# Kernel optimization log

Measured on AMD Instinct MI355X. Metric: run time of the kernel, lower is better.

Reference implementation:

```python
import jax, jax.numpy as jnp
import numpy as np

N = 50000   # nodes
E = 800000  # edges (before self-loops)
IN, HID, OUT = 128, 128, 64


def gcn_norm(edge_index, num_nodes):
    # add self loops with weight 1, then symmetric deg^-1/2 normalization
    loop = jnp.arange(num_nodes, dtype=edge_index.dtype)
    row = jnp.concatenate([edge_index[0], loop])
    col = jnp.concatenate([edge_index[1], loop])
    ew = jnp.ones(row.shape[0], dtype=jnp.float32)
    deg = jax.ops.segment_sum(ew, col, num_segments=num_nodes)
    dis = jnp.where(deg > 0, jax.lax.rsqrt(deg), 0.0)
    norm = dis[row] * ew * dis[col]
    return row, col, norm


def gcn_conv(x, row, col, norm, W, b):
    h = x @ W                                   # [N, F_out] dense GEMM
    msg = h[row] * norm[:, None]                # gather + scale over edges
    out = jax.ops.segment_sum(msg, col, num_segments=x.shape[0])  # scatter-add
    return out + b


def setup_inputs() -> dict:
    key = jax.random.key(0)
    k0, k1, k2, k3, k4, k5 = jax.random.split(key, 6)
    x = jax.random.normal(k0, (N, IN), dtype=jnp.float32)
    edge_index = jax.random.randint(k1, (2, E), 0, N, dtype=jnp.int32)
    # glorot-style init for linear weights, zeros for bias (PyG default)
    W1 = jax.random.normal(k2, (IN, HID), dtype=jnp.float32) * np.float32(np.sqrt(1.0 / IN))
    b1 = jnp.zeros((HID,), dtype=jnp.float32)
    W2 = jax.random.normal(k3, (HID, OUT), dtype=jnp.float32) * np.float32(np.sqrt(1.0 / HID))
    b2 = jnp.zeros((OUT,), dtype=jnp.float32)
    return {"x": x, "edge_index": edge_index, "W1": W1, "b1": b1, "W2": W2, "b2": b2}


def reference(x, edge_index, W1, b1, W2, b2):
    row, col, norm = gcn_norm(edge_index, x.shape[0])
    h = jax.nn.relu(gcn_conv(x, row, col, norm, W1, b1))
    # dropout is a no-op in eval mode (training=False)
    out = gcn_conv(h, row, col, norm, W2, b2)
    return out
```

## Files before the change

kernel.cpp:

```cpp
#include <hip/hip_runtime.h>
#include <hip/hip_fp16.h>


#define Nn 50000
#define Ne 800000
#define SCAN_B ((Nn + 1023) / 1024)

using f16x8 = _Float16 __attribute__((ext_vector_type(8)));
using f32x4 = float __attribute__((ext_vector_type(4)));

__global__ __launch_bounds__(256) void k_count(const int* __restrict__ col,
                                               int* __restrict__ degi,
                                               unsigned short* __restrict__ rank) {
  int e = blockIdx.x * 256 + threadIdx.x;
  if (e < Ne) rank[e] = (unsigned short)atomicAdd(&degi[col[e]], 1);
}

__global__ __launch_bounds__(1024) void k_scan1(const int* __restrict__ degi,
                                                int* __restrict__ rowptr,
                                                float* __restrict__ dis,
                                                int* __restrict__ bsum) {
  __shared__ int wsum[16];
  int tid = threadIdx.x;
  int lane = tid & 63, wid = tid >> 6;
  int i = blockIdx.x * 1024 + tid;
  int v = (i < Nn) ? degi[i] : 0;
  if (i < Nn) dis[i] = rsqrtf((float)(v + 1));
  int incl = v;
  #pragma unroll
  for (int off = 1; off < 64; off <<= 1) {
    int t = __shfl_up(incl, off);
    if (lane >= off) incl += t;
  }
  if (lane == 63) wsum[wid] = incl;
  __syncthreads();
  if (wid == 0) {
    int wv = (lane < 16) ? wsum[lane] : 0;
    #pragma unroll
    for (int off = 1; off < 16; off <<= 1) {
      int t = __shfl_up(wv, off);
      if (lane >= off) wv += t;
    }
    if (lane < 16) wsum[lane] = wv;
  }
  __syncthreads();
  int woff = (wid > 0) ? wsum[wid - 1] : 0;
  if (i < Nn) rowptr[i] = woff + incl - v;
  if (tid == 0) bsum[blockIdx.x] = wsum[15];
}

__global__ __launch_bounds__(64) void k_scan2(int* __restrict__ bsum,
                                              int* __restrict__ rowptr) {
  int lane = threadIdx.x;
  int v = (lane < SCAN_B) ? bsum[lane] : 0;
  int incl = v;
  #pragma unroll
  for (int off = 1; off < 64; off <<= 1) {
    int t = __shfl_up(incl, off);
    if (lane >= off) incl += t;
  }
  if (lane < SCAN_B) bsum[lane] = incl - v;
  if (lane == 63) rowptr[Nn] = incl;
}

__global__ __launch_bounds__(1024) void k_scan3(int* __restrict__ rowptr,
                                                const int* __restrict__ bsum) {
  int i = blockIdx.x * 1024 + threadIdx.x;
  if (i < Nn) rowptr[i] += bsum[blockIdx.x];
}

__global__ __launch_bounds__(256) void k_fill(const int* __restrict__ row,
                                              const int* __restrict__ col,
                                              const float* __restrict__ dis,
                                              const int* __restrict__ rowptr,
                                              const unsigned short* __restrict__ rank,
                                              unsigned int* __restrict__ csr) {
  int e = blockIdx.x * 256 + threadIdx.x;
  if (e >= Ne) return;
  int r = row[e], c = col[e];
  int pos = rowptr[c] + (int)rank[e];
  __half hn = __float2half(dis[r] * dis[c]);
  csr[pos] = ((unsigned int)__half_as_ushort(hn) << 16) | (unsigned int)r;
}

template <int LDO>
__global__ __launch_bounds__(256) void k_gemm_mfma(const float* __restrict__ X,
                                                   const float* __restrict__ W,
                                                   __half* __restrict__ H, int n) {
  __shared__ _Float16 Xs[64 * 136];
  __shared__ _Float16 Wts[LDO * 136];
  const int tid = threadIdx.x;
  const int base = blockIdx.x * 64;

  {
    constexpr int C4 = LDO / 4;
    for (int idx4 = tid; idx4 < 32 * LDO; idx4 += 256) {
      int k = idx4 / C4;
      int c = (idx4 % C4) * 4;
      float4 wv = ((const float4*)W)[idx4];
      Wts[(c + 0) * 136 + k] = (_Float16)wv.x;
      Wts[(c + 1) * 136 + k] = (_Float16)wv.y;
      Wts[(c + 2) * 136 + k] = (_Float16)wv.z;
      Wts[(c + 3) * 136 + k] = (_Float16)wv.w;
    }
  }
  {
    for (int u = tid; u < 64 * 16; u += 256) {
      int r = u >> 4, seg = u & 15;
      int node = base + r;
      if (node >= n) node = n - 1;
      const float4* xg = (const float4*)(X + (size_t)node * 128 + seg * 8);
      float4 x0 = xg[0], x1 = xg[1];
      f16x8 hv;
      hv[0] = (_Float16)x0.x; hv[1] = (_Float16)x0.y;
      hv[2] = (_Float16)x0.z; hv[3] = (_Float16)x0.w;
      hv[4] = (_Float16)x1.x; hv[5] = (_Float16)x1.y;
      hv[6] = (_Float16)x1.z; hv[7] = (_Float16)x1.w;
      *(f16x8*)&Xs[r * 136 + seg * 8] = hv;
    }
  }
  __syncthreads();

  const int w = tid >> 6, lane = tid & 63;
  const int quad = lane >> 4, mrow = lane & 15;
  constexpr int NCT = LDO / 16;

  f32x4 acc[NCT];
  #pragma unroll
  for (int ct = 0; ct < NCT; ++ct) acc[ct] = (f32x4){0.f, 0.f, 0.f, 0.f};

  #pragma unroll
  for (int ko = 0; ko < 4; ++ko) {
    f16x8 av = *(const f16x8*)&Xs[(w * 16 + mrow) * 136 + ko * 32 + quad * 8];
    #pragma unroll
    for (int ct = 0; ct < NCT; ++ct) {
      f16x8 bv = *(const f16x8*)&Wts[(ct * 16 + mrow) * 136 + ko * 32 + quad * 8];
      acc[ct] = __builtin_amdgcn_mfma_f32_16x16x32_f16(av, bv, acc[ct], 0, 0, 0);
    }
  }

  #pragma unroll
  for (int ct = 0; ct < NCT; ++ct) {
    #pragma unroll
    for (int r = 0; r < 4; ++r) {
      int node = base + w * 16 + quad * 4 + r;
      if (node < n)
        H[(size_t)node * LDO + ct * 16 + mrow] = __float2half(acc[ct][r]);
    }
  }
}

__device__ __forceinline__ float2 h2f(unsigned int u) {
  return __half22float2(*(const __half2*)&u);
}
__device__ __forceinline__ float wdec(unsigned int u) {
  return __half2float(__ushort_as_half((unsigned short)(u >> 16)));
}

__global__ __launch_bounds__(256) void k_agg128(const __half* __restrict__ H,
                                                const unsigned int* __restrict__ csr,
                                                const int* __restrict__ rowptr,
                                                const float* __restrict__ dis,
                                                const float* __restrict__ bias,
                                                float* __restrict__ Out, int n) {
  const int wid = threadIdx.x >> 6, lane = threadIdx.x & 63;
  const int sub = lane >> 4, fl = lane & 15;
  int v = blockIdx.x * 16 + wid * 4 + sub;
  if (v >= n) return;
  int s = rowptr[v], e = rowptr[v + 1];
  float d = dis[v];
  float sw = d * d;
  const uint4* Hq = (const uint4*)H;
  uint4 hv = Hq[(size_t)v * 16 + fl];
  float2 p0 = h2f(hv.x), p1 = h2f(hv.y), p2 = h2f(hv.z), p3 = h2f(hv.w);
  float a0 = p0.x * sw, a1 = p0.y * sw, a2 = p1.x * sw, a3 = p1.y * sw;
  float a4 = p2.x * sw, a5 = p2.y * sw, a6 = p3.x * sw, a7 = p3.y * sw;
  int i = s;
  for (; i + 4 <= e; i += 4) {
    unsigned int u0 = csr[i + 0], u1 = csr[i + 1];
    unsigned int u2 = csr[i + 2], u3 = csr[i + 3];
    uint4 q0 = Hq[(size_t)(u0 & 0xFFFFu) * 16 + fl];
    uint4 q1 = Hq[(size_t)(u1 & 0xFFFFu) * 16 + fl];
    uint4 q2 = Hq[(size_t)(u2 & 0xFFFFu) * 16 + fl];
    uint4 q3 = Hq[(size_t)(u3 & 0xFFFFu) * 16 + fl];
    float w0 = wdec(u0), w1 = wdec(u1), w2 = wdec(u2), w3 = wdec(u3);
    float2 t;
    t = h2f(q0.x); a0 = fmaf(w0, t.x, a0); a1 = fmaf(w0, t.y, a1);
    t = h2f(q0.y); a2 = fmaf(w0, t.x, a2); a3 = fmaf(w0, t.y, a3);
    t = h2f(q0.z); a4 = fmaf(w0, t.x, a4); a5 = fmaf(w0, t.y, a5);
    t = h2f(q0.w); a6 = fmaf(w0, t.x, a6); a7 = fmaf(w0, t.y, a7);
    t = h2f(q1.x); a0 = fmaf(w1, t.x, a0); a1 = fmaf(w1, t.y, a1);
    t = h2f(q1.y); a2 = fmaf(w1, t.x, a2); a3 = fmaf(w1, t.y, a3);
    t = h2f(q1.z); a4 = fmaf(w1, t.x, a4); a5 = fmaf(w1, t.y, a5);
    t = h2f(q1.w); a6 = fmaf(w1, t.x, a6); a7 = fmaf(w1, t.y, a7);
    t = h2f(q2.x); a0 = fmaf(w2, t.x, a0); a1 = fmaf(w2, t.y, a1);
    t = h2f(q2.y); a2 = fmaf(w2, t.x, a2); a3 = fmaf(w2, t.y, a3);
    t = h2f(q2.z); a4 = fmaf(w2, t.x, a4); a5 = fmaf(w2, t.y, a5);
    t = h2f(q2.w); a6 = fmaf(w2, t.x, a6); a7 = fmaf(w2, t.y, a7);
    t = h2f(q3.x); a0 = fmaf(w3, t.x, a0); a1 = fmaf(w3, t.y, a1);
    t = h2f(q3.y); a2 = fmaf(w3, t.x, a2); a3 = fmaf(w3, t.y, a3);
    t = h2f(q3.z); a4 = fmaf(w3, t.x, a4); a5 = fmaf(w3, t.y, a5);
    t = h2f(q3.w); a6 = fmaf(w3, t.x, a6); a7 = fmaf(w3, t.y, a7);
  }
  for (; i < e; ++i) {
    unsigned int u = csr[i];
    uint4 q = Hq[(size_t)(u & 0xFFFFu) * 16 + fl];
    float w = wdec(u);
    float2 t;
    t = h2f(q.x); a0 = fmaf(w, t.x, a0); a1 = fmaf(w, t.y, a1);
    t = h2f(q.y); a2 = fmaf(w, t.x, a2); a3 = fmaf(w, t.y, a3);
    t = h2f(q.z); a4 = fmaf(w, t.x, a4); a5 = fmaf(w, t.y, a5);
    t = h2f(q.w); a6 = fmaf(w, t.x, a6); a7 = fmaf(w, t.y, a7);
  }
  const float4* Bq = (const float4*)bias;
  float4 b0 = Bq[fl * 2], b1 = Bq[fl * 2 + 1];
  float4 o0 = make_float4(fmaxf(a0 + b0.x, 0.f), fmaxf(a1 + b0.y, 0.f),
                          fmaxf(a2 + b0.z, 0.f), fmaxf(a3 + b0.w, 0.f));
  float4 o1 = make_float4(fmaxf(a4 + b1.x, 0.f), fmaxf(a5 + b1.y, 0.f),
                          fmaxf(a6 + b1.z, 0.f), fmaxf(a7 + b1.w, 0.f));
  float4* Oq = (float4*)(Out + (size_t)v * 128);
  Oq[fl * 2] = o0;
  Oq[fl * 2 + 1] = o1;
}

__global__ __launch_bounds__(256) void k_agg64(const __half* __restrict__ H,
                                               const unsigned int* __restrict__ csr,
                                               const int* __restrict__ rowptr,
                                               const float* __restrict__ dis,
                                               const float* __restrict__ bias,
                                               float* __restrict__ Out, int n) {
  const int wid = threadIdx.x >> 6, lane = threadIdx.x & 63;
  const int sub = lane >> 4, fl = lane & 15;
  int v = blockIdx.x * 16 + wid * 4 + sub;
  if (v >= n) return;
  int s = rowptr[v], e = rowptr[v + 1];
  float d = dis[v];
  float sw = d * d;
  const uint2* Hq = (const uint2*)H;
  uint2 hv = Hq[(size_t)v * 16 + fl];
  float2 p0 = h2f(hv.x), p1 = h2f(hv.y);
  float a0 = p0.x * sw, a1 = p0.y * sw, a2 = p1.x * sw, a3 = p1.y * sw;
  int i = s;
  for (; i + 4 <= e; i += 4) {
    unsigned int u0 = csr[i + 0], u1 = csr[i + 1];
    unsigned int u2 = csr[i + 2], u3 = csr[i + 3];
    uint2 q0 = Hq[(size_t)(u0 & 0xFFFFu) * 16 + fl];
    uint2 q1 = Hq[(size_t)(u1 & 0xFFFFu) * 16 + fl];
    uint2 q2 = Hq[(size_t)(u2 & 0xFFFFu) * 16 + fl];
    uint2 q3 = Hq[(size_t)(u3 & 0xFFFFu) * 16 + fl];
    float w0 = wdec(u0), w1 = wdec(u1), w2 = wdec(u2), w3 = wdec(u3);
    float2 t;
    t = h2f(q0.x); a0 = fmaf(w0, t.x, a0); a1 = fmaf(w0, t.y, a1);
    t = h2f(q0.y); a2 = fmaf(w0, t.x, a2); a3 = fmaf(w0, t.y, a3);
    t = h2f(q1.x); a0 = fmaf(w1, t.x, a0); a1 = fmaf(w1, t.y, a1);
    t = h2f(q1.y); a2 = fmaf(w1, t.x, a2); a3 = fmaf(w1, t.y, a3);
    t = h2f(q2.x); a0 = fmaf(w2, t.x, a0); a1 = fmaf(w2, t.y, a1);
    t = h2f(q2.y); a2 = fmaf(w2, t.x, a2); a3 = fmaf(w2, t.y, a3);
    t = h2f(q3.x); a0 = fmaf(w3, t.x, a0); a1 = fmaf(w3, t.y, a1);
    t = h2f(q3.y); a2 = fmaf(w3, t.x, a2); a3 = fmaf(w3, t.y, a3);
  }
  for (; i < e; ++i) {
    unsigned int u = csr[i];
    uint2 q = Hq[(size_t)(u & 0xFFFFu) * 16 + fl];
    float w = wdec(u);
    float2 t;
    t = h2f(q.x); a0 = fmaf(w, t.x, a0); a1 = fmaf(w, t.y, a1);
    t = h2f(q.y); a2 = fmaf(w, t.x, a2); a3 = fmaf(w, t.y, a3);
  }
  const float4* Bq = (const float4*)bias;
  float4 b = Bq[fl];
  float4 o = make_float4(a0 + b.x, a1 + b.y, a2 + b.z, a3 + b.w);
  ((float4*)(Out + (size_t)v * 64))[fl] = o;
}

extern "C" void kernel_launch(void* const* d_in, const int* in_sizes, int n_in,
                              void* d_out, int out_size, void* d_ws, size_t ws_size,
                              hipStream_t stream) {
  const float* x  = (const float*)d_in[0];
  const int*   ei = (const int*)d_in[1];
  const int*   row = ei;
  const int*   col = ei + Ne;
  const float* W1 = (const float*)d_in[2];
  const float* b1 = (const float*)d_in[3];
  const float* W2 = (const float*)d_in[4];
  const float* b2 = (const float*)d_in[5];
  float* out = (float*)d_out;

  char* ws = (char*)d_ws;
  size_t off = 0;
  auto alloc = [&](size_t bytes) -> void* {
    void* p = ws + off;
    off += (bytes + 255) & ~(size_t)255;
    return p;
  };
  int*    degi   = (int*)   alloc(Nn * sizeof(int));
  int*    rowptr = (int*)   alloc((Nn + 1) * sizeof(int));
  float*  dis    = (float*) alloc(Nn * sizeof(float));
  int*    bsum   = (int*)   alloc(64 * sizeof(int));
  unsigned short* rank = (unsigned short*)alloc((size_t)Ne * sizeof(unsigned short));
  unsigned int* csr = (unsigned int*)alloc((size_t)Ne * sizeof(unsigned int));
  __half* H1     = (__half*)alloc((size_t)Nn * 128 * sizeof(__half));
  float*  H1b    = (float*) alloc((size_t)Nn * 128 * sizeof(float));
  __half* H2     = (__half*)alloc((size_t)Nn * 64 * sizeof(__half));

  hipMemsetAsync(degi, 0, Nn * sizeof(int), stream);

  const int EB  = (Ne + 255) / 256;
  const int NGB = (Nn + 15) / 16;
  const int GT  = (Nn + 63) / 64;

  k_count<<<EB, 256, 0, stream>>>(col, degi, rank);
  k_scan1<<<SCAN_B, 1024, 0, stream>>>(degi, rowptr, dis, bsum);
  k_scan2<<<1, 64, 0, stream>>>(bsum, rowptr);
  k_scan3<<<SCAN_B, 1024, 0, stream>>>(rowptr, bsum);
  k_fill<<<EB, 256, 0, stream>>>(row, col, dis, rowptr, rank, csr);

  k_gemm_mfma<128><<<GT, 256, 0, stream>>>(x, W1, H1, Nn);
  k_agg128<<<NGB, 256, 0, stream>>>(H1, csr, rowptr, dis, b1, H1b, Nn);

  k_gemm_mfma<64><<<GT, 256, 0, stream>>>(H1b, W2, H2, Nn);
  k_agg64<<<NGB, 256, 0, stream>>>(H2, csr, rowptr, dis, b2, out, Nn);
}
```

Baseline: 221.4 us.

## Shrink CSR to 16-bit indices, fuse scan kernels, deepen gather batching

The CSR entries become 16-bit source indices. Edge weights are no longer stored per edge; the aggregation recomputes them as dis[src]*dis[dst], which halves CSR traffic and removes the dis gathers from the fill kernel. The separate block-offset scan kernel is merged into scan3, with each block redoing the small 64-wide scan itself, so one launch goes away. The aggregation loops now issue 6 or 8 independent gathers per batch and handle the tail with a single predicated batch, giving more memory-level parallelism. The cost is an extra random dis load per edge and more registers per thread.

```diff
diff --git a/kernel.cpp b/kernel.cpp
--- a/kernel.cpp
+++ b/kernel.cpp
@@ -49,38 +49,35 @@
   if (tid == 0) bsum[blockIdx.x] = wsum[15];
 }
 
-__global__ __launch_bounds__(64) void k_scan2(int* __restrict__ bsum,
-                                              int* __restrict__ rowptr) {
-  int lane = threadIdx.x;
-  int v = (lane < SCAN_B) ? bsum[lane] : 0;
-  int incl = v;
-  #pragma unroll
-  for (int off = 1; off < 64; off <<= 1) {
-    int t = __shfl_up(incl, off);
-    if (lane >= off) incl += t;
-  }
-  if (lane < SCAN_B) bsum[lane] = incl - v;
-  if (lane == 63) rowptr[Nn] = incl;
-}
-
 __global__ __launch_bounds__(1024) void k_scan3(int* __restrict__ rowptr,
                                                 const int* __restrict__ bsum) {
-  int i = blockIdx.x * 1024 + threadIdx.x;
-  if (i < Nn) rowptr[i] += bsum[blockIdx.x];
+  __shared__ int off_s;
+  int tid = threadIdx.x;
+  if (tid < 64) {
+    int v = (tid < SCAN_B) ? bsum[tid] : 0;
+    int incl = v;
+    #pragma unroll
+    for (int off = 1; off < 64; off <<= 1) {
+      int t = __shfl_up(incl, off);
+      if (tid >= off) incl += t;
+    }
+    if (tid == (int)blockIdx.x) off_s = incl - v;
+    if (blockIdx.x == 0 && tid == SCAN_B - 1) rowptr[Nn] = incl;
+  }
+  __syncthreads();
+  int i = blockIdx.x * 1024 + tid;
+  if (i < Nn) rowptr[i] += off_s;
 }
 
 __global__ __launch_bounds__(256) void k_fill(const int* __restrict__ row,
                                               const int* __restrict__ col,
-                                              const float* __restrict__ dis,
                                               const int* __restrict__ rowptr,
                                               const unsigned short* __restrict__ rank,
-                                              unsigned int* __restrict__ csr) {
+                                              unsigned short* __restrict__ csr) {
   int e = blockIdx.x * 256 + threadIdx.x;
   if (e >= Ne) return;
   int r = row[e], c = col[e];
-  int pos = rowptr[c] + (int)rank[e];
-  __half hn = __float2half(dis[r] * dis[c]);
-  csr[pos] = ((unsigned int)__half_as_ushort(hn) << 16) | (unsigned int)r;
+  csr[rowptr[c] + (int)rank[e]] = (unsigned short)r;
 }
 
 template <int LDO>
@@ -153,12 +150,9 @@
 __device__ __forceinline__ float2 h2f(unsigned int u) {
   return __half22float2(*(const __half2*)&u);
 }
-__device__ __forceinline__ float wdec(unsigned int u) {
-  return __half2float(__ushort_as_half((unsigned short)(u >> 16)));
-}
 
 __global__ __launch_bounds__(256) void k_agg128(const __half* __restrict__ H,
-                                                const unsigned int* __restrict__ csr,
+                                                const unsigned short* __restrict__ csr,
                                                 const int* __restrict__ rowptr,
                                                 const float* __restrict__ dis,
                                                 const float* __restrict__ bias,
@@ -175,42 +169,50 @@
   float2 p0 = h2f(hv.x), p1 = h2f(hv.y), p2 = h2f(hv.z), p3 = h2f(hv.w);
   float a0 = p0.x * sw, a1 = p0.y * sw, a2 = p1.x * sw, a3 = p1.y * sw;
   float a4 = p2.x * sw, a5 = p2.y * sw, a6 = p3.x * sw, a7 = p3.y * sw;
+  constexpr int D = 6;
   int i = s;
-  for (; i + 4 <= e; i += 4) {
-    unsigned int u0 = csr[i + 0], u1 = csr[i + 1];
-    unsigned int u2 = csr[i + 2], u3 = csr[i + 3];
-    uint4 q0 = Hq[(size_t)(u0 & 0xFFFFu) * 16 + fl];
-    uint4 q1 = Hq[(size_t)(u1 & 0xFFFFu) * 16 + fl];
-    uint4 q2 = Hq[(size_t)(u2 & 0xFFFFu) * 16 + fl];
-    uint4 q3 = Hq[(size_t)(u3 & 0xFFFFu) * 16 + fl];
-    float w0 = wdec(u0), w1 = wdec(u1), w2 = wdec(u2), w3 = wdec(u3);
-    float2 t;
-    t = h2f(q0.x); a0 = fmaf(w0, t.x, a0); a1 = fmaf(w0, t.y, a1);
-    t = h2f(q0.y); a2 = fmaf(w0, t.x, a2); a3 = fmaf(w0, t.y, a3);
-    t = h2f(q0.z); a4 = fmaf(w0, t.x, a4); a5 = fmaf(w0, t.y, a5);
-    t = h2f(q0.w); a6 = fmaf(w0, t.x, a6); a7 = fmaf(w0, t.y, a7);
-    t = h2f(q1.x); a0 = fmaf(w1, t.x, a0); a1 = fmaf(w1, t.y, a1);
-    t = h2f(q1.y); a2 = fmaf(w1, t.x, a2); a3 = fmaf(w1, t.y, a3);
-    t = h2f(q1.z); a4 = fmaf(w1, t.x, a4); a5 = fmaf(w1, t.y, a5);
-    t = h2f(q1.w); a6 = fmaf(w1, t.x, a6); a7 = fmaf(w1, t.y, a7);
-    t = h2f(q2.x); a0 = fmaf(w2, t.x, a0); a1 = fmaf(w2, t.y, a1);
-    t = h2f(q2.y); a2 = fmaf(w2, t.x, a2); a3 = fmaf(w2, t.y, a3);
-    t = h2f(q2.z); a4 = fmaf(w2, t.x, a4); a5 = fmaf(w2, t.y, a5);
-    t = h2f(q2.w); a6 = fmaf(w2, t.x, a6); a7 = fmaf(w2, t.y, a7);
-    t = h2f(q3.x); a0 = fmaf(w3, t.x, a0); a1 = fmaf(w3, t.y, a1);
-    t = h2f(q3.y); a2 = fmaf(w3, t.x, a2); a3 = fmaf(w3, t.y, a3);
-    t = h2f(q3.z); a4 = fmaf(w3, t.x, a4); a5 = fmaf(w3, t.y, a5);
-    t = h2f(q3.w); a6 = fmaf(w3, t.x, a6); a7 = fmaf(w3, t.y, a7);
-  }
-  for (; i < e; ++i) {
-    unsigned int u = csr[i];
-    uint4 q = Hq[(size_t)(u & 0xFFFFu) * 16 + fl];
-    float w = wdec(u);
-    float2 t;
-    t = h2f(q.x); a0 = fmaf(w, t.x, a0); a1 = fmaf(w, t.y, a1);
-    t = h2f(q.y); a2 = fmaf(w, t.x, a2); a3 = fmaf(w, t.y, a3);
-    t = h2f(q.z); a4 = fmaf(w, t.x, a4); a5 = fmaf(w, t.y, a5);
-    t = h2f(q.w); a6 = fmaf(w, t.x, a6); a7 = fmaf(w, t.y, a7);
+  for (; i + D <= e; i += D) {
+    int srcs[D];
+    uint4 q[D];
+    float wd[D];
+    #pragma unroll
+    for (int j = 0; j < D; ++j) srcs[j] = csr[i + j];
+    #pragma unroll
+    for (int j = 0; j < D; ++j) q[j] = Hq[(size_t)srcs[j] * 16 + fl];
+    #pragma unroll
+    for (int j = 0; j < D; ++j) wd[j] = dis[srcs[j]];
+    #pragma unroll
+    for (int j = 0; j < D; ++j) {
+      float w = wd[j] * d;
+      float2 t;
+      t = h2f(q[j].x); a0 = fmaf(w, t.x, a0); a1 = fmaf(w, t.y, a1);
+      t = h2f(q[j].y); a2 = fmaf(w, t.x, a2); a3 = fmaf(w, t.y, a3);
+      t = h2f(q[j].z); a4 = fmaf(w, t.x, a4); a5 = fmaf(w, t.y, a5);
+      t = h2f(q[j].w); a6 = fmaf(w, t.x, a6); a7 = fmaf(w, t.y, a7);
+    }
+  }
+  if (i < e) {
+    int srcs[D];
+    uint4 q[D];
+    float wd[D];
+    #pragma unroll
+    for (int j = 0; j < D; ++j) {
+      int idx = (i + j < e) ? i + j : e - 1;
+      srcs[j] = csr[idx];
+    }
+    #pragma unroll
+    for (int j = 0; j < D; ++j) q[j] = Hq[(size_t)srcs[j] * 16 + fl];
+    #pragma unroll
+    for (int j = 0; j < D; ++j) wd[j] = dis[srcs[j]];
+    #pragma unroll
+    for (int j = 0; j < D; ++j) {
+      float w = (i + j < e) ? wd[j] * d : 0.f;
+      float2 t;
+      t = h2f(q[j].x); a0 = fmaf(w, t.x, a0); a1 = fmaf(w, t.y, a1);
+      t = h2f(q[j].y); a2 = fmaf(w, t.x, a2); a3 = fmaf(w, t.y, a3);
+      t = h2f(q[j].z); a4 = fmaf(w, t.x, a4); a5 = fmaf(w, t.y, a5);
+      t = h2f(q[j].w); a6 = fmaf(w, t.x, a6); a7 = fmaf(w, t.y, a7);
+    }
   }
   const float4* Bq = (const float4*)bias;
   float4 b0 = Bq[fl * 2], b1 = Bq[fl * 2 + 1];
@@ -224,7 +226,7 @@
 }
 
 __global__ __launch_bounds__(256) void k_agg64(const __half* __restrict__ H,
-                                               const unsigned int* __restrict__ csr,
+                                               const unsigned short* __restrict__ csr,
                                                const int* __restrict__ rowptr,
                                                const float* __restrict__ dis,
                                                const float* __restrict__ bias,
@@ -240,32 +242,46 @@
   uint2 hv = Hq[(size_t)v * 16 + fl];
   float2 p0 = h2f(hv.x), p1 = h2f(hv.y);
   float a0 = p0.x * sw, a1 = p0.y * sw, a2 = p1.x * sw, a3 = p1.y * sw;
+  constexpr int D = 8;
   int i = s;
-  for (; i + 4 <= e; i += 4) {
-    unsigned int u0 = csr[i + 0], u1 = csr[i + 1];
-    unsigned int u2 = csr[i + 2], u3 = csr[i + 3];
-    uint2 q0 = Hq[(size_t)(u0 & 0xFFFFu) * 16 + fl];
-    uint2 q1 = Hq[(size_t)(u1 & 0xFFFFu) * 16 + fl];
-    uint2 q2 = Hq[(size_t)(u2 & 0xFFFFu) * 16 + fl];
-    uint2 q3 = Hq[(size_t)(u3 & 0xFFFFu) * 16 + fl];
-    float w0 = wdec(u0), w1 = wdec(u1), w2 = wdec(u2), w3 = wdec(u3);
-    float2 t;
-    t = h2f(q0.x); a0 = fmaf(w0, t.x, a0); a1 = fmaf(w0, t.y, a1);
-    t = h2f(q0.y); a2 = fmaf(w0, t.x, a2); a3 = fmaf(w0, t.y, a3);
-    t = h2f(q1.x); a0 = fmaf(w1, t.x, a0); a1 = fmaf(w1, t.y, a1);
-    t = h2f(q1.y); a2 = fmaf(w1, t.x, a2); a3 = fmaf(w1, t.y, a3);
-    t = h2f(q2.x); a0 = fmaf(w2, t.x, a0); a1 = fmaf(w2, t.y, a1);
-    t = h2f(q2.y); a2 = fmaf(w2, t.x, a2); a3 = fmaf(w2, t.y, a3);
-    t = h2f(q3.x); a0 = fmaf(w3, t.x, a0); a1 = fmaf(w3, t.y, a1);
-    t = h2f(q3.y); a2 = fmaf(w3, t.x, a2); a3 = fmaf(w3, t.y, a3);
-  }
-  for (; i < e; ++i) {
-    unsigned int u = csr[i];
-    uint2 q = Hq[(size_t)(u & 0xFFFFu) * 16 + fl];
-    float w = wdec(u);
-    float2 t;
-    t = h2f(q.x); a0 = fmaf(w, t.x, a0); a1 = fmaf(w, t.y, a1);
-    t = h2f(q.y); a2 = fmaf(w, t.x, a2); a3 = fmaf(w, t.y, a3);
+  for (; i + D <= e; i += D) {
+    int srcs[D];
+    uint2 q[D];
+    float wd[D];
+    #pragma unroll
+    for (int j = 0; j < D; ++j) srcs[j] = csr[i + j];
+    #pragma unroll
+    for (int j = 0; j < D; ++j) q[j] = Hq[(size_t)srcs[j] * 16 + fl];
+    #pragma unroll
+    for (int j = 0; j < D; ++j) wd[j] = dis[srcs[j]];
+    #pragma unroll
+    for (int j = 0; j < D; ++j) {
+      float w = wd[j] * d;
+      float2 t;
+      t = h2f(q[j].x); a0 = fmaf(w, t.x, a0); a1 = fmaf(w, t.y, a1);
+      t = h2f(q[j].y); a2 = fmaf(w, t.x, a2); a3 = fmaf(w, t.y, a3);
+    }
+  }
+  if (i < e) {
+    int srcs[D];
+    uint2 q[D];
+    float wd[D];
+    #pragma unroll
+    for (int j = 0; j < D; ++j) {
+      int idx = (i + j < e) ? i + j : e - 1;
+      srcs[j] = csr[idx];
+    }
+    #pragma unroll
+    for (int j = 0; j < D; ++j) q[j] = Hq[(size_t)srcs[j] * 16 + fl];
+    #pragma unroll
+    for (int j = 0; j < D; ++j) wd[j] = dis[srcs[j]];
+    #pragma unroll
+    for (int j = 0; j < D; ++j) {
+      float w = (i + j < e) ? wd[j] * d : 0.f;
+      float2 t;
+      t = h2f(q[j].x); a0 = fmaf(w, t.x, a0); a1 = fmaf(w, t.y, a1);
+      t = h2f(q[j].y); a2 = fmaf(w, t.x, a2); a3 = fmaf(w, t.y, a3);
+    }
   }
   const float4* Bq = (const float4*)bias;
   float4 b = Bq[fl];
@@ -298,7 +314,7 @@
   float*  dis    = (float*) alloc(Nn * sizeof(float));
   int*    bsum   = (int*)   alloc(64 * sizeof(int));
   unsigned short* rank = (unsigned short*)alloc((size_t)Ne * sizeof(unsigned short));
-  unsigned int* csr = (unsigned int*)alloc((size_t)Ne * sizeof(unsigned int));
+  unsigned short* csr  = (unsigned short*)alloc((size_t)Ne * sizeof(unsigned short));
   __half* H1     = (__half*)alloc((size_t)Nn * 128 * sizeof(__half));
   float*  H1b    = (float*) alloc((size_t)Nn * 128 * sizeof(float));
   __half* H2     = (__half*)alloc((size_t)Nn * 64 * sizeof(__half));
@@ -311,9 +327,8 @@
 
   k_count<<<EB, 256, 0, stream>>>(col, degi, rank);
   k_scan1<<<SCAN_B, 1024, 0, stream>>>(degi, rowptr, dis, bsum);
-  k_scan2<<<1, 64, 0, stream>>>(bsum, rowptr);
   k_scan3<<<SCAN_B, 1024, 0, stream>>>(rowptr, bsum);
-  k_fill<<<EB, 256, 0, stream>>>(row, col, dis, rowptr, rank, csr);
+  k_fill<<<EB, 256, 0, stream>>>(row, col, rowptr, rank, csr);
 
   k_gemm_mfma<128><<<GT, 256, 0, stream>>>(x, W1, H1, Nn);
   k_agg128<<<NGB, 256, 0, stream>>>(H1, csr, rowptr, dis, b1, H1b, Nn);
```

New measurement: 211.3 us. -4.6%, faster.
